# Performance work log

Measured on AMD Instinct MI355X. Metric: run time of the kernel, lower is better.

## Reference

```python
import jax, jax.numpy as jnp
import numpy as np

B, L = 128, 200
NUM_C, D, M = 10000, 128, 64


def setup_inputs() -> dict:
    key = jax.random.key(0)
    ks = jax.random.split(key, 16)
    n = lambda k, s, sc=0.05: jax.random.normal(k, s, dtype=jnp.float32) * sc
    return {
        "q": jax.random.randint(ks[0], (B, L), 0, NUM_C),
        "r": jax.random.randint(ks[1], (B, L), 0, 2),
        "k_emb": n(ks[2], (NUM_C, D)),
        "v_emb": n(ks[3], (2, D)),
        "Mk": n(ks[4], (M, D), 0.2),   # kaiming_normal_
        "Mv0": n(ks[5], (M, D), 0.2),  # kaiming_normal_
        "f_W": n(ks[6], (D, 2 * D)), "f_b": jnp.zeros((D,), jnp.float32),
        "e_W": n(ks[7], (D, D)), "e_b": jnp.zeros((D,), jnp.float32),
        "a_W": n(ks[8], (D, D)), "a_b": jnp.zeros((D,), jnp.float32),
        "ab_W": n(ks[9], (1, D)), "ab_b": jnp.zeros((1,), jnp.float32),
        "df_W": n(ks[10], (1, D)), "df_b": jnp.zeros((1,), jnp.float32),
    }


def reference(q, r, k_emb, v_emb, Mk, Mv0, f_W, f_b, e_W, e_b, a_W, a_b, ab_W, ab_b, df_W, df_b):
    # Embeddings
    k = k_emb[q]                # [B, L, D] question key embedding
    v = k + v_emb[r]            # [B, L, D] value embedding

    # Attention over memory slots, erase/add gates
    w = jax.nn.softmax(jnp.einsum('bld,md->blm', k, Mk), axis=-1)   # [B, L, M]
    e = jax.nn.sigmoid(jnp.einsum('bld,ed->ble', v, e_W) + e_b)      # erase [B, L, D]
    a = jnp.tanh(jnp.einsum('bld,ed->ble', v, a_W) + a_b)            # add   [B, L, D]

    Mvt0 = jnp.broadcast_to(Mv0[None], (q.shape[0], Mv0.shape[0], Mv0.shape[1]))  # [B, M, D]

    def step(Mvt, inp):
        wt, et, at = inp  # [B,M], [B,D], [B,D]
        # read uses memory BEFORE this timestep's write (Mv[:, :-1] in torch)
        read = jnp.einsum('bm,bmd->bd', wt, Mvt)
        we = wt[:, :, None]
        Mvt_new = Mvt * (1.0 - we * et[:, None, :]) + we * at[:, None, :]
        return Mvt_new, read

    _, reads = jax.lax.scan(
        step, Mvt0,
        (w.transpose(1, 0, 2), e.transpose(1, 0, 2), a.transpose(1, 0, 2)))
    reads = reads.transpose(1, 0, 2)  # [B, L, D]

    f = jnp.tanh(jnp.concatenate([reads, k], axis=-1) @ f_W.T + f_b)  # [B, L, D]
    stu_ability = jnp.tanh(f @ ab_W.T + ab_b)   # [B, L, 1] (dropout is identity in eval)
    que_diff = jnp.tanh(k @ df_W.T + df_b)      # [B, L, 1]
    p = jax.nn.sigmoid(3.0 * stu_ability - que_diff)
    return p.squeeze(-1)  # [B, L]
```

## Files before the change

kernel.cpp:

```cpp
#include <hip/hip_runtime.h>

typedef unsigned short ushort_t;
typedef unsigned int uint_t;
typedef short bf16x8 __attribute__((ext_vector_type(8)));
typedef float f32x4 __attribute__((ext_vector_type(4)));

#define B_ 128
#define L_ 200
#define D_ 128
#define M_ 64

__device__ __forceinline__ float fast_sigmoid(float x) {
    return 1.f / (1.f + __expf(-x));
}

__device__ __forceinline__ float fast_tanh(float x) {
    float xc = fminf(fmaxf(x, -15.f), 15.f);
    float e = __expf(2.f * xc);
    return (e - 1.f) / (e + 1.f);
}

__device__ __forceinline__ float bf2f(ushort_t h) {
    union { unsigned int u; float f; } x;
    x.u = ((unsigned int)h) << 16;
    return x.f;
}

__device__ __forceinline__ float asf(uint_t u) {
    union { unsigned int u; float f; } x;
    x.u = u;
    return x.f;
}

__device__ __forceinline__ ushort_t f2bf(float f) {
    union { float f; unsigned int u; } x;
    x.f = f;
    unsigned int u = x.u;
    unsigned int r = (u + 0x7FFFu + ((u >> 16) & 1u)) >> 16;
    return (ushort_t)r;
}

__device__ __forceinline__ uint4 pack8(float4 a, float4 b) {
    uint4 u;
    u.x = (unsigned)f2bf(a.x) | ((unsigned)f2bf(a.y) << 16);
    u.y = (unsigned)f2bf(a.z) | ((unsigned)f2bf(a.w) << 16);
    u.z = (unsigned)f2bf(b.x) | ((unsigned)f2bf(b.y) << 16);
    u.w = (unsigned)f2bf(b.z) | ((unsigned)f2bf(b.w) << 16);
    return u;
}

#define F_WQ   0u
#define F_EAQ  1638400u
#define F_FKQ  8192000u
#define F_RD   11468800u
#define F_DIFF 14745600u
#define F_PACK 14771200u
#define WPACK_N 57344
#define FPACK_N 16384

__global__ __launch_bounds__(256) void k_pack(
    const float* __restrict__ Mk, const float* __restrict__ eW,
    const float* __restrict__ aW, const float* __restrict__ fW,
    ushort_t* __restrict__ Wpack, ushort_t* __restrict__ Fpack)
{
    int i = blockIdx.x * 256 + threadIdx.x;
    if (i < WPACK_N) {
        int g = i >> 9, lane = (i >> 3) & 63, j = i & 7;
        int nt = g >> 2, ks = g & 3;
        int col = nt * 16 + (lane & 15);
        int d = ks * 32 + ((lane >> 4) << 3) + j;
        float v;
        if (col < 64)       v = Mk[col * 128 + d];
        else if (col < 192) v = eW[(col - 64) * 128 + d];
        else if (col < 320) v = aW[(col - 192) * 128 + d];
        else                v = fW[(col - 320) * 256 + 128 + d];
        Wpack[i] = f2bf(v);
    } else if (i < WPACK_N + FPACK_N) {
        int e = i - WPACK_N;
        int g = e >> 9, lane = (e >> 3) & 63, j = e & 7;
        int nt = g >> 2, ks = g & 3;
        int col = nt * 16 + (lane & 15);
        int d = ks * 32 + ((lane >> 4) << 3) + j;
        Fpack[e] = f2bf(fW[col * 256 + d]);
    }
}

__device__ __forceinline__ void loadB4(const ushort_t* __restrict__ base,
                                       int nt, int lane, bf16x8* b) {
    const ushort_t* p = base + (nt * 256 + lane) * 8;
    b[0] = *(const bf16x8*)(p);
    b[1] = *(const bf16x8*)(p + 512);
    b[2] = *(const bf16x8*)(p + 1024);
    b[3] = *(const bf16x8*)(p + 1536);
}

__global__ __launch_bounds__(512) void k_pre_mfma(
    const int* __restrict__ q, const int* __restrict__ r,
    const float* __restrict__ k_emb, const float* __restrict__ v_emb,
    const ushort_t* __restrict__ Wpack,
    const float* __restrict__ e_b, const float* __restrict__ a_b,
    const float* __restrict__ df_W, const float* __restrict__ df_b,
    ushort_t* __restrict__ wq, uint_t* __restrict__ eaq,
    float* __restrict__ fkq, float* __restrict__ diffq)
{
    __shared__ ushort_t skA[8192];
    __shared__ ushort_t svA[8192];
    __shared__ float slog[64 * 68];

    const int tid = threadIdx.x;
    const int pos0 = blockIdx.x * 64;
    const int wave = tid >> 6;
    const int lane = tid & 63;
    const int mt = wave & 3;
    const int nh = wave >> 2;

    #pragma unroll
    for (int i = 0; i < 2; i++) {
        int E = tid + 512 * i;
        int mtile = E >> 8, ks = (E >> 6) & 3, le = E & 63;
        int prow = pos0 + mtile * 16 + (le & 15);
        int dof = ks * 32 + ((le >> 4) << 3);
        int qv = q[prow], rv = r[prow];
        const float4* kp = (const float4*)(k_emb + qv * 128 + dof);
        float4 ka = kp[0], kb = kp[1];
        const float4* vp = (const float4*)(v_emb + rv * 128 + dof);
        float4 va = vp[0], vb = vp[1];
        *(uint4*)&skA[E * 8] = pack8(ka, kb);
        float4 s0, s1;
        s0.x = ka.x + va.x; s0.y = ka.y + va.y; s0.z = ka.z + va.z; s0.w = ka.w + va.w;
        s1.x = kb.x + vb.x; s1.y = kb.y + vb.y; s1.z = kb.z + vb.z; s1.w = kb.w + vb.w;
        *(uint4*)&svA[E * 8] = pack8(s0, s1);
    }
    __syncthreads();

    bf16x8 A[4];
    {
        const ushort_t* src = nh ? svA : skA;
        #pragma unroll
        for (int ks = 0; ks < 4; ks++)
            A[ks] = *(const bf16x8*)&src[((mt * 4 + ks) * 64 + lane) * 8];
    }

    const int col = lane & 15;
    const int quad = lane >> 4;
    const int rbase = mt * 16 + quad * 4;

    if (nh == 0) {
        bf16x8 Bb[2][4];
        loadB4(Wpack, 0, lane, Bb[0]);
        #pragma unroll
        for (int j = 0; j < 12; j++) {
            if (j < 11) {
                int jn = j + 1;
                loadB4(Wpack, (jn < 4) ? jn : jn + 16, lane, Bb[jn & 1]);
            }
            f32x4 acc = {0.f, 0.f, 0.f, 0.f};
            #pragma unroll
            for (int ks = 0; ks < 4; ks++)
                acc = __builtin_amdgcn_mfma_f32_16x16x32_bf16(A[ks], Bb[j & 1][ks], acc, 0, 0, 0);
            if (j < 4) {
                #pragma unroll
                for (int reg = 0; reg < 4; reg++)
                    slog[(rbase + reg) * 68 + j * 16 + col] = acc[reg];
            } else {
                int c = (j - 4) * 16 + col;
                #pragma unroll
                for (int reg = 0; reg < 4; reg++)
                    fkq[(pos0 + rbase + reg) * 128 + c] = acc[reg];
            }
        }
        {
            int row = tid >> 2, ln = tid & 3;
            const float* lr = slog + row * 68 + ln * 16;
            float v[16];
            #pragma unroll
            for (int j = 0; j < 16; j++) v[j] = lr[j];
            float mx = v[0];
            #pragma unroll
            for (int j = 1; j < 16; j++) mx = fmaxf(mx, v[j]);
            mx = fmaxf(mx, __shfl_xor(mx, 1));
            mx = fmaxf(mx, __shfl_xor(mx, 2));
            float s = 0.f;
            #pragma unroll
            for (int j = 0; j < 16; j++) { v[j] = __expf(v[j] - mx); s += v[j]; }
            s += __shfl_xor(s, 1); s += __shfl_xor(s, 2);
            float inv = 1.f / s;
            uint4 u0, u1;
            u0.x = (unsigned)f2bf(v[0] * inv)  | ((unsigned)f2bf(v[1] * inv) << 16);
            u0.y = (unsigned)f2bf(v[2] * inv)  | ((unsigned)f2bf(v[3] * inv) << 16);
            u0.z = (unsigned)f2bf(v[4] * inv)  | ((unsigned)f2bf(v[5] * inv) << 16);
            u0.w = (unsigned)f2bf(v[6] * inv)  | ((unsigned)f2bf(v[7] * inv) << 16);
            u1.x = (unsigned)f2bf(v[8] * inv)  | ((unsigned)f2bf(v[9] * inv) << 16);
            u1.y = (unsigned)f2bf(v[10] * inv) | ((unsigned)f2bf(v[11] * inv) << 16);
            u1.z = (unsigned)f2bf(v[12] * inv) | ((unsigned)f2bf(v[13] * inv) << 16);
            u1.w = (unsigned)f2bf(v[14] * inv) | ((unsigned)f2bf(v[15] * inv) << 16);
            uint4* wout = (uint4*)(wq + (pos0 + row) * 64 + ln * 16);
            wout[0] = u0;
            wout[1] = u1;
        }
    } else {
        bf16x8 Be[2][4], Ba[2][4];
        loadB4(Wpack, 4, lane, Be[0]);
        loadB4(Wpack, 12, lane, Ba[0]);
        #pragma unroll
        for (int i = 0; i < 8; i++) {
            if (i < 7) {
                loadB4(Wpack, 5 + i, lane, Be[(i + 1) & 1]);
                loadB4(Wpack, 13 + i, lane, Ba[(i + 1) & 1]);
            }
            f32x4 ae = {0.f, 0.f, 0.f, 0.f};
            f32x4 aa = {0.f, 0.f, 0.f, 0.f};
            #pragma unroll
            for (int ks = 0; ks < 4; ks++) {
                ae = __builtin_amdgcn_mfma_f32_16x16x32_bf16(A[ks], Be[i & 1][ks], ae, 0, 0, 0);
                aa = __builtin_amdgcn_mfma_f32_16x16x32_bf16(A[ks], Ba[i & 1][ks], aa, 0, 0, 0);
            }
            int c = i * 16 + col;
            float ebv = e_b[c], abv = a_b[c];
            #pragma unroll
            for (int reg = 0; reg < 4; reg++) {
                float ev = fast_sigmoid(ae[reg] + ebv);
                float av = fast_tanh(aa[reg] + abv);
                eaq[(pos0 + rbase + reg) * 128 + c] =
                    (unsigned)f2bf(ev) | ((unsigned)f2bf(av) << 16);
            }
        }
        {
            int t2 = tid - 256;
            int row = t2 >> 2, ks = t2 & 3;
            int mtile = row >> 4, rowin = row & 15;
            float s = 0.f;
            #pragma unroll
            for (int q8 = 0; q8 < 4; q8++) {
                bf16x8 kv = *(const bf16x8*)&skA[((mtile * 4 + ks) * 64 + (q8 * 16 + rowin)) * 8];
                const float* dfp = df_W + ks * 32 + q8 * 8;
                #pragma unroll
                for (int j = 0; j < 8; j++)
                    s = fmaf(bf2f((ushort_t)kv[j]), dfp[j], s);
            }
            s += __shfl_xor(s, 1); s += __shfl_xor(s, 2);
            if (ks == 0) diffq[pos0 + row] = fast_tanh(s + df_b[0]);
        }
    }
}

#define SC_PRE(wX, eX, cN)                                                 \
    _Pragma("unroll")                                                      \
    for (int tt = 0; tt < 8; tt++) {                                       \
        wX[tt] = *(const uint4*)(wb + ((cN) * 8 + tt) * 64);               \
        eX[tt] = eab[((cN) * 8 + tt) * 128];                               \
    }

#define SC_CMP(wX, eX, cN)                                                 \
    _Pragma("unroll")                                                      \
    for (int tt = 0; tt < 8; tt++) {                                       \
        uint4 wu = wX[tt];                                                 \
        uint_t eu = eX[tt];                                                \
        float ev = asf(eu << 16), av = asf(eu & 0xFFFF0000u), ne = -ev;    \
        float g0 = asf(wu.x << 16), g1 = asf(wu.x & 0xFFFF0000u);          \
        float g2 = asf(wu.y << 16), g3 = asf(wu.y & 0xFFFF0000u);          \
        float g4 = asf(wu.z << 16), g5 = asf(wu.z & 0xFFFF0000u);          \
        float g6 = asf(wu.w << 16), g7 = asf(wu.w & 0xFFFF0000u);          \
        float r0, r1;                                                      \
        r0 = g0 * Mv[0];                                                   \
        r1 = g1 * Mv[1];                                                   \
        r0 = fmaf(g2, Mv[2], r0); r1 = fmaf(g3, Mv[3], r1);                \
        r0 = fmaf(g4, Mv[4], r0); r1 = fmaf(g5, Mv[5], r1);                \
        r0 = fmaf(g6, Mv[6], r0); r1 = fmaf(g7, Mv[7], r1);                \
        Mv[0] = fmaf(g0, fmaf(ne, Mv[0], av), Mv[0]);                      \
        Mv[1] = fmaf(g1, fmaf(ne, Mv[1], av), Mv[1]);                      \
        Mv[2] = fmaf(g2, fmaf(ne, Mv[2], av), Mv[2]);                      \
        Mv[3] = fmaf(g3, fmaf(ne, Mv[3], av), Mv[3]);                      \
        Mv[4] = fmaf(g4, fmaf(ne, Mv[4], av), Mv[4]);                      \
        Mv[5] = fmaf(g5, fmaf(ne, Mv[5], av), Mv[5]);                      \
        Mv[6] = fmaf(g6, fmaf(ne, Mv[6], av), Mv[6]);                      \
        Mv[7] = fmaf(g7, fmaf(ne, Mv[7], av), Mv[7]);                      \
        float rd = r0 + r1;                                                \
        rd += __shfl_xor(rd, 8);                                           \
        rd += __shfl_xor(rd, 16);                                          \
        rd += __shfl_xor(rd, 32);                                          \
        if (s == 0) {                                                      \
            int pos = pos_base + (cN) * 8 + tt;                            \
            int idx = (((pos >> 4) * 4 + ksd) * 64                         \
                       + (q8d * 16 + (pos & 15))) * 8 + jd;                \
            rdpack[idx] = f2bf(rd);                                        \
        }                                                                  \
    }

__global__ __launch_bounds__(256) void k_scan(
    const ushort_t* __restrict__ wq, const uint_t* __restrict__ eaq,
    const float* __restrict__ Mv0, ushort_t* __restrict__ rdpack)
{
    const int tid = threadIdx.x;
    const int b = blockIdx.x >> 2;
    const int dq = blockIdx.x & 3;
    const int wv = tid >> 6;
    const int lane = tid & 63;
    const int s = lane >> 3;
    const int dl = lane & 7;
    const int d = dq * 32 + wv * 8 + dl;

    float Mv[8];
    #pragma unroll
    for (int j = 0; j < 8; j++) Mv[j] = Mv0[(s * 8 + j) * D_ + d];

    const ushort_t* wb = wq + b * (L_ * M_) + s * 8;
    const uint_t* eab = eaq + b * (L_ * 128) + d;

    const int pos_base = b * L_;
    const int ksd = d >> 5;
    const int q8d = (d >> 3) & 3;
    const int jd = d & 7;

    uint4 wA[8], wB[8];
    uint_t eA[8], eB[8];

    SC_PRE(wA, eA, 0);
    for (int c = 0; c < 12; c++) {
        SC_PRE(wB, eB, 2 * c + 1);
        SC_CMP(wA, eA, 2 * c);
        SC_PRE(wA, eA, 2 * c + 2);
        SC_CMP(wB, eB, 2 * c + 1);
    }
    SC_CMP(wA, eA, 24);
}

__global__ __launch_bounds__(512) void k_final_mfma(
    const ushort_t* __restrict__ rdpack, const float* __restrict__ fkq,
    const float* __restrict__ diffq, const ushort_t* __restrict__ Fpack,
    const float* __restrict__ f_b, const float* __restrict__ ab_W,
    const float* __restrict__ ab_b, float* __restrict__ out)
{
    __shared__ float sab[64 * 2];

    const int tid = threadIdx.x;
    const int pos0 = blockIdx.x * 64;
    const int wave = tid >> 6;
    const int lane = tid & 63;
    const int mt = wave & 3;
    const int half = wave >> 2;

    const int col = lane & 15;
    const int quad = lane >> 4;
    const int rbase = mt * 16 + quad * 4;

    bf16x8 A[4];
    {
        const ushort_t* rp = rdpack + (blockIdx.x * 4 + mt) * 2048 + lane * 8;
        #pragma unroll
        for (int ks = 0; ks < 4; ks++)
            A[ks] = *(const bf16x8*)(rp + ks * 512);
    }

    float fkv[16];
    #pragma unroll
    for (int i = 0; i < 4; i++)
        #pragma unroll
        for (int reg = 0; reg < 4; reg++)
            fkv[i * 4 + reg] = fkq[(pos0 + rbase + reg) * 128 + (half * 4 + i) * 16 + col];

    float abacc[4] = {0.f, 0.f, 0.f, 0.f};

    bf16x8 Bb[2][4];
    loadB4(Fpack, half * 4, lane, Bb[0]);
    #pragma unroll
    for (int i = 0; i < 4; i++) {
        if (i < 3) loadB4(Fpack, half * 4 + i + 1, lane, Bb[(i + 1) & 1]);
        f32x4 acc = {0.f, 0.f, 0.f, 0.f};
        #pragma unroll
        for (int ks = 0; ks < 4; ks++)
            acc = __builtin_amdgcn_mfma_f32_16x16x32_bf16(A[ks], Bb[i & 1][ks], acc, 0, 0, 0);
        int c = (half * 4 + i) * 16 + col;
        float fb = f_b[c];
        float abw = ab_W[c];
        #pragma unroll
        for (int reg = 0; reg < 4; reg++) {
            float fv = fast_tanh(acc[reg] + fkv[i * 4 + reg] + fb);
            abacc[reg] = fmaf(abw, fv, abacc[reg]);
        }
    }

    #pragma unroll
    for (int reg = 0; reg < 4; reg++) {
        float v = abacc[reg];
        v += __shfl_xor(v, 1); v += __shfl_xor(v, 2);
        v += __shfl_xor(v, 4); v += __shfl_xor(v, 8);
        abacc[reg] = v;
    }
    if (col == 0) {
        #pragma unroll
        for (int reg = 0; reg < 4; reg++)
            sab[(rbase + reg) * 2 + half] = abacc[reg];
    }
    __syncthreads();
    if (tid < 64) {
        float ab = fast_tanh(sab[tid * 2] + sab[tid * 2 + 1] + ab_b[0]);
        int pos = pos0 + tid;
        out[pos] = fast_sigmoid(3.f * ab - diffq[pos]);
    }
}

extern "C" void kernel_launch(void* const* d_in, const int* in_sizes, int n_in,
                              void* d_out, int out_size, void* d_ws, size_t ws_size,
                              hipStream_t stream)
{
    const int*   q     = (const int*)d_in[0];
    const int*   r     = (const int*)d_in[1];
    const float* k_emb = (const float*)d_in[2];
    const float* v_emb = (const float*)d_in[3];
    const float* Mk    = (const float*)d_in[4];
    const float* Mv0   = (const float*)d_in[5];
    const float* f_W   = (const float*)d_in[6];
    const float* f_b   = (const float*)d_in[7];
    const float* e_W   = (const float*)d_in[8];
    const float* e_b   = (const float*)d_in[9];
    const float* a_W   = (const float*)d_in[10];
    const float* a_b   = (const float*)d_in[11];
    const float* ab_W  = (const float*)d_in[12];
    const float* ab_b  = (const float*)d_in[13];
    const float* df_W  = (const float*)d_in[14];
    const float* df_b  = (const float*)d_in[15];

    float* ws = (float*)d_ws;
    float* out = (float*)d_out;
    ushort_t* wq = (ushort_t*)(ws + F_WQ);
    uint_t* eaq = (uint_t*)(ws + F_EAQ);
    ushort_t* Wpack = (ushort_t*)(ws + F_PACK);
    ushort_t* Fpack = Wpack + WPACK_N;
    ushort_t* rdpack = (ushort_t*)(ws + F_RD);

    k_pack<<<288, 256, 0, stream>>>(Mk, e_W, a_W, f_W, Wpack, Fpack);

    k_pre_mfma<<<400, 512, 0, stream>>>(
        q, r, k_emb, v_emb, Wpack, e_b, a_b, df_W, df_b,
        wq, eaq, ws + F_FKQ, ws + F_DIFF);

    k_scan<<<512, 256, 0, stream>>>(wq, eaq, Mv0, rdpack);

    k_final_mfma<<<400, 512, 0, stream>>>(
        rdpack, ws + F_FKQ, ws + F_DIFF, Fpack,
        f_b, ab_W, ab_b, out);
}
```

Baseline: 157.7 us.

## Halve per-thread scan slots to double scan blocks; load embeddings directly into MFMA regs

The scan kernel now gives each thread 4 memory slots instead of 8 and covers 16 D-columns per block instead of 32, doubling the grid to 1024 blocks, with an extra shuffle step in the read reduction. This is meant to raise parallelism and occupancy for the latency-bound sequential scan, at the cost of more shuffles and more redundant w loads per step. The pre kernel also drops its LDS staging of gathered embeddings: waves gather and pack the A fragments straight from global memory, and the difficulty dot product is computed in fp32 from k_emb. That removes a barrier and LDS traffic but issues more scattered global loads.

```diff
diff --git a/kernel.cpp b/kernel.cpp
--- a/kernel.cpp
+++ b/kernel.cpp
@@ -18,12 +18,6 @@
     float xc = fminf(fmaxf(x, -15.f), 15.f);
     float e = __expf(2.f * xc);
     return (e - 1.f) / (e + 1.f);
-}
-
-__device__ __forceinline__ float bf2f(ushort_t h) {
-    union { unsigned int u; float f; } x;
-    x.u = ((unsigned int)h) << 16;
-    return x.f;
 }
 
 __device__ __forceinline__ float asf(uint_t u) {
@@ -103,8 +97,6 @@
     ushort_t* __restrict__ wq, uint_t* __restrict__ eaq,
     float* __restrict__ fkq, float* __restrict__ diffq)
 {
-    __shared__ ushort_t skA[8192];
-    __shared__ ushort_t svA[8192];
     __shared__ float slog[64 * 68];
 
     const int tid = threadIdx.x;
@@ -114,36 +106,38 @@
     const int mt = wave & 3;
     const int nh = wave >> 2;
 
-    #pragma unroll
-    for (int i = 0; i < 2; i++) {
-        int E = tid + 512 * i;
-        int mtile = E >> 8, ks = (E >> 6) & 3, le = E & 63;
-        int prow = pos0 + mtile * 16 + (le & 15);
-        int dof = ks * 32 + ((le >> 4) << 3);
-        int qv = q[prow], rv = r[prow];
-        const float4* kp = (const float4*)(k_emb + qv * 128 + dof);
-        float4 ka = kp[0], kb = kp[1];
-        const float4* vp = (const float4*)(v_emb + rv * 128 + dof);
-        float4 va = vp[0], vb = vp[1];
-        *(uint4*)&skA[E * 8] = pack8(ka, kb);
-        float4 s0, s1;
-        s0.x = ka.x + va.x; s0.y = ka.y + va.y; s0.z = ka.z + va.z; s0.w = ka.w + va.w;
-        s1.x = kb.x + vb.x; s1.y = kb.y + vb.y; s1.z = kb.z + vb.z; s1.w = kb.w + vb.w;
-        *(uint4*)&svA[E * 8] = pack8(s0, s1);
-    }
-    __syncthreads();
-
-    bf16x8 A[4];
-    {
-        const ushort_t* src = nh ? svA : skA;
-        #pragma unroll
-        for (int ks = 0; ks < 4; ks++)
-            A[ks] = *(const bf16x8*)&src[((mt * 4 + ks) * 64 + lane) * 8];
-    }
-
     const int col = lane & 15;
     const int quad = lane >> 4;
     const int rbase = mt * 16 + quad * 4;
+
+    bf16x8 A[4];
+    {
+        const int arow = pos0 + mt * 16 + col;
+        const int qv = q[arow];
+        const float4* kp = (const float4*)(k_emb + qv * 128) + quad * 2;
+        if (nh == 0) {
+            #pragma unroll
+            for (int ks = 0; ks < 4; ks++) {
+                uint4 u = pack8(kp[ks * 8], kp[ks * 8 + 1]);
+                A[ks] = *(bf16x8*)&u;
+            }
+        } else {
+            const int rv = r[arow];
+            const float4* vp = (const float4*)(v_emb + rv * 128) + quad * 2;
+            #pragma unroll
+            for (int ks = 0; ks < 4; ks++) {
+                float4 x0 = kp[ks * 8], x1 = kp[ks * 8 + 1];
+                float4 y0 = vp[ks * 8], y1 = vp[ks * 8 + 1];
+                float4 s0, s1;
+                s0.x = x0.x + y0.x; s0.y = x0.y + y0.y;
+                s0.z = x0.z + y0.z; s0.w = x0.w + y0.w;
+                s1.x = x1.x + y1.x; s1.y = x1.y + y1.y;
+                s1.z = x1.z + y1.z; s1.w = x1.w + y1.w;
+                uint4 u = pack8(s0, s1);
+                A[ks] = *(bf16x8*)&u;
+            }
+        }
+    }
 
     if (nh == 0) {
         bf16x8 Bb[2][4];
@@ -227,19 +221,19 @@
         }
         {
             int t2 = tid - 256;
-            int row = t2 >> 2, ks = t2 & 3;
-            int mtile = row >> 4, rowin = row & 15;
+            int row = t2 >> 2, ln = t2 & 3;
+            int pos = pos0 + row;
+            int qv = q[pos];
+            const float4* kp = (const float4*)(k_emb + qv * 128) + ln * 8;
+            const float4* dfp = (const float4*)df_W + ln * 8;
             float s = 0.f;
             #pragma unroll
-            for (int q8 = 0; q8 < 4; q8++) {
-                bf16x8 kv = *(const bf16x8*)&skA[((mtile * 4 + ks) * 64 + (q8 * 16 + rowin)) * 8];
-                const float* dfp = df_W + ks * 32 + q8 * 8;
-                #pragma unroll
-                for (int j = 0; j < 8; j++)
-                    s = fmaf(bf2f((ushort_t)kv[j]), dfp[j], s);
+            for (int j = 0; j < 8; j++) {
+                float4 a = kp[j], b = dfp[j];
+                s = fmaf(a.x, b.x, fmaf(a.y, b.y, fmaf(a.z, b.z, fmaf(a.w, b.w, s))));
             }
             s += __shfl_xor(s, 1); s += __shfl_xor(s, 2);
-            if (ks == 0) diffq[pos0 + row] = fast_tanh(s + df_b[0]);
+            if (ln == 0) diffq[pos] = fast_tanh(s + df_b[0]);
         }
     }
 }
@@ -247,35 +241,28 @@
 #define SC_PRE(wX, eX, cN)                                                 \
     _Pragma("unroll")                                                      \
     for (int tt = 0; tt < 8; tt++) {                                       \
-        wX[tt] = *(const uint4*)(wb + ((cN) * 8 + tt) * 64);               \
+        wX[tt] = *(const uint2*)(wb + ((cN) * 8 + tt) * 64);               \
         eX[tt] = eab[((cN) * 8 + tt) * 128];                               \
     }
 
 #define SC_CMP(wX, eX, cN)                                                 \
     _Pragma("unroll")                                                      \
     for (int tt = 0; tt < 8; tt++) {                                       \
-        uint4 wu = wX[tt];                                                 \
+        uint2 wu = wX[tt];                                                 \
         uint_t eu = eX[tt];                                                \
         float ev = asf(eu << 16), av = asf(eu & 0xFFFF0000u), ne = -ev;    \
         float g0 = asf(wu.x << 16), g1 = asf(wu.x & 0xFFFF0000u);          \
         float g2 = asf(wu.y << 16), g3 = asf(wu.y & 0xFFFF0000u);          \
-        float g4 = asf(wu.z << 16), g5 = asf(wu.z & 0xFFFF0000u);          \
-        float g6 = asf(wu.w << 16), g7 = asf(wu.w & 0xFFFF0000u);          \
         float r0, r1;                                                      \
         r0 = g0 * Mv[0];                                                   \
         r1 = g1 * Mv[1];                                                   \
         r0 = fmaf(g2, Mv[2], r0); r1 = fmaf(g3, Mv[3], r1);                \
-        r0 = fmaf(g4, Mv[4], r0); r1 = fmaf(g5, Mv[5], r1);                \
-        r0 = fmaf(g6, Mv[6], r0); r1 = fmaf(g7, Mv[7], r1);                \
         Mv[0] = fmaf(g0, fmaf(ne, Mv[0], av), Mv[0]);                      \
         Mv[1] = fmaf(g1, fmaf(ne, Mv[1], av), Mv[1]);                      \
         Mv[2] = fmaf(g2, fmaf(ne, Mv[2], av), Mv[2]);                      \
         Mv[3] = fmaf(g3, fmaf(ne, Mv[3], av), Mv[3]);                      \
-        Mv[4] = fmaf(g4, fmaf(ne, Mv[4], av), Mv[4]);                      \
-        Mv[5] = fmaf(g5, fmaf(ne, Mv[5], av), Mv[5]);                      \
-        Mv[6] = fmaf(g6, fmaf(ne, Mv[6], av), Mv[6]);                      \
-        Mv[7] = fmaf(g7, fmaf(ne, Mv[7], av), Mv[7]);                      \
         float rd = r0 + r1;                                                \
+        rd += __shfl_xor(rd, 4);                                           \
         rd += __shfl_xor(rd, 8);                                           \
         rd += __shfl_xor(rd, 16);                                          \
         rd += __shfl_xor(rd, 32);                                          \
@@ -292,19 +279,19 @@
     const float* __restrict__ Mv0, ushort_t* __restrict__ rdpack)
 {
     const int tid = threadIdx.x;
-    const int b = blockIdx.x >> 2;
-    const int dq = blockIdx.x & 3;
+    const int b = blockIdx.x >> 3;
+    const int dq = blockIdx.x & 7;
     const int wv = tid >> 6;
     const int lane = tid & 63;
-    const int s = lane >> 3;
-    const int dl = lane & 7;
-    const int d = dq * 32 + wv * 8 + dl;
-
-    float Mv[8];
+    const int s = lane >> 2;
+    const int dl = lane & 3;
+    const int d = dq * 16 + wv * 4 + dl;
+
+    float Mv[4];
     #pragma unroll
-    for (int j = 0; j < 8; j++) Mv[j] = Mv0[(s * 8 + j) * D_ + d];
-
-    const ushort_t* wb = wq + b * (L_ * M_) + s * 8;
+    for (int j = 0; j < 4; j++) Mv[j] = Mv0[(s * 4 + j) * D_ + d];
+
+    const ushort_t* wb = wq + b * (L_ * M_) + s * 4;
     const uint_t* eab = eaq + b * (L_ * 128) + d;
 
     const int pos_base = b * L_;
@@ -312,7 +299,7 @@
     const int q8d = (d >> 3) & 3;
     const int jd = d & 7;
 
-    uint4 wA[8], wB[8];
+    uint2 wA[8], wB[8];
     uint_t eA[8], eB[8];
 
     SC_PRE(wA, eA, 0);
@@ -435,7 +422,7 @@
         q, r, k_emb, v_emb, Wpack, e_b, a_b, df_W, df_b,
         wq, eaq, ws + F_FKQ, ws + F_DIFF);
 
-    k_scan<<<512, 256, 0, stream>>>(wq, eaq, Mv0, rdpack);
+    k_scan<<<1024, 256, 0, stream>>>(wq, eaq, Mv0, rdpack);
 
     k_final_mfma<<<400, 512, 0, stream>>>(
         rdpack, ws + F_FKQ, ws + F_DIFF, Fpack,
```

Result: slower. 173.1 us (+9.8%).
